# Performance work log

Hardware: AMD Instinct MI355X
Metric: run time of the kernel (lower is better)

Reference implementation:

```python
import jax, jax.numpy as jnp
import numpy as np

B, N, D = 512, 131072, 256
N_BAGS, GRID = 64, 96
DIS_THRESHOLD = 2.0
TEMP = 0.2


def setup_inputs() -> dict:
    key = jax.random.key(0)
    k = jax.random.split(key, 8)
    q = jax.random.normal(k[0], (B, D), dtype=jnp.float32)
    memory = jax.random.normal(k[1], (N, D), dtype=jnp.float32)
    # memory bank holds L2-normalized features (MoCo-style)
    memory = memory / jnp.linalg.norm(memory, axis=1, keepdims=True)
    bag_idx = jax.random.randint(k[2], (B,), 0, N_BAGS, dtype=jnp.int32)
    x_coord = jax.random.randint(k[3], (B,), 0, GRID, dtype=jnp.int32)
    y_coord = jax.random.randint(k[4], (B,), 0, GRID, dtype=jnp.int32)
    bag_idxs = jax.random.randint(k[5], (N,), 0, N_BAGS, dtype=jnp.int32)
    x_coords = jax.random.randint(k[6], (N,), 0, GRID, dtype=jnp.int32)
    y_coords = jax.random.randint(k[7], (N,), 0, GRID, dtype=jnp.int32)
    return {"q": q, "memory": memory, "bag_idx": bag_idx,
            "x_coord": x_coord, "y_coord": y_coord,
            "bag_idxs": bag_idxs, "x_coords": x_coords, "y_coords": y_coords}


def _spatial_pos(q, memory, bag_idx, x_coord, y_coord, bag_idxs, x_coords, y_coords):
    # q = F.normalize(neck(backbone(img))[0])
    qn = q / jnp.linalg.norm(q, axis=1, keepdims=True)
    # l_all = einsum('bc,cn', q, memory.T); s_all = exp(l_all / 0.2)
    l_all = jnp.einsum("bc,nc->bn", qn, memory)  # [B, N]
    s_all = jnp.exp(l_all / TEMP)
    # chosen_patch_idx: same bag as query
    chosen = bag_idx[:, None] == bag_idxs[None, :]  # [B, N] bool
    # cdist(coords, coords_bank, p=2) via squared-distance expansion
    # (coords are small integers -> exact in fp32; compare d^2 against thr^2 / 0)
    cq = jnp.stack((x_coord, y_coord), axis=1).astype(jnp.float32)   # [B, 2]
    cb = jnp.stack((x_coords, y_coords), axis=1).astype(jnp.float32)  # [N, 2]
    d2 = (jnp.sum(cq * cq, axis=1)[:, None]
          + jnp.sum(cb * cb, axis=1)[None, :]
          - 2.0 * cq @ cb.T)  # [B, N]
    near = (d2 < DIS_THRESHOLD * DIS_THRESHOLD) & (d2 > 0.0)
    pos_idx = chosen & near
    # s_pos_spatial = sum(where(pos_idx, s_all, 0), dim=1)
    s_pos_spatial = jnp.sum(jnp.where(pos_idx, s_all, 0.0), axis=1)  # [B]
    return s_pos_spatial, pos_idx


def reference(q, memory, bag_idx, x_coord, y_coord, bag_idxs, x_coords, y_coords):
    s_pos_spatial, _ = _spatial_pos(q, memory, bag_idx, x_coord, y_coord,
                                    bag_idxs, x_coords, y_coords)
    return s_pos_spatial
```

## Files before the change

kernel.cpp:

```cpp
#include <hip/hip_runtime.h>
#include <math.h>

#define NBAGS  64
#define BAGCAP 40
#define TBL    (BAGCAP * NBAGS)
#define D4     64

__global__ void __launch_bounds__(256)
k_fused(const float* __restrict__ q,
        const float* __restrict__ memory,
        const int* __restrict__ bag_idx,
        const int* __restrict__ x_coord,
        const int* __restrict__ y_coord,
        const int* __restrict__ bag_idxs,
        const int* __restrict__ x_coords,
        const int* __restrict__ y_coords,
        float* __restrict__ out,
        int B, int N)
{
    __shared__ int s_cnt[NBAGS];
    __shared__ int s_tbl[TBL];
    int tid = threadIdx.x;
    if (tid < NBAGS) s_cnt[tid] = 0;
    __syncthreads();

    for (int i = tid; i < B; i += 256) {
        int bag  = bag_idx[i];
        int slot = atomicAdd(&s_cnt[bag], 1);
        if (slot < BAGCAP)
            s_tbl[slot * NBAGS + bag] = (i << 14) | (x_coord[i] << 7) | y_coord[i];
    }
    __syncthreads();

    int j = blockIdx.x * 256 + tid;
    if (j >= N) return;

    int jb = bag_idxs[j];
    int jx = x_coords[j];
    int jy = y_coords[j];
    int n  = min(s_cnt[jb], BAGCAP);

    const float4* q4 = (const float4*)q;
    const float4* m4 = (const float4*)memory;

    for (int i = 0; i < n; ++i) {
        int e  = s_tbl[i * NBAGS + jb];
        int dx = ((e >> 7) & 127) - jx;
        int dy = (e & 127) - jy;
        int d2 = dx * dx + dy * dy;
        if (d2 > 0 && d2 < 4) {
            int b = e >> 14;
            const float4* qr = q4 + b * D4;
            const float4* mr = m4 + (long)j * D4;
            float qq = 0.0f, qm = 0.0f;
            #pragma unroll 8
            for (int k = 0; k < D4; ++k) {
                float4 a = qr[k];
                float4 m = mr[k];
                qq += a.x * a.x + a.y * a.y + a.z * a.z + a.w * a.w;
                qm += a.x * m.x + a.y * m.y + a.z * m.z + a.w * m.w;
            }
            float l = qm / sqrtf(qq);
            atomicAdd(&out[b], expf(l * 5.0f));
        }
    }
}

extern "C" void kernel_launch(void* const* d_in, const int* in_sizes, int n_in,
                              void* d_out, int out_size, void* d_ws, size_t ws_size,
                              hipStream_t stream)
{
    const float* q        = (const float*)d_in[0];
    const float* memory   = (const float*)d_in[1];
    const int*   bag_idx  = (const int*)d_in[2];
    const int*   x_coord  = (const int*)d_in[3];
    const int*   y_coord  = (const int*)d_in[4];
    const int*   bag_idxs = (const int*)d_in[5];
    const int*   x_coords = (const int*)d_in[6];
    const int*   y_coords = (const int*)d_in[7];
    float*       out      = (float*)d_out;

    int B = in_sizes[2];
    int N = in_sizes[5];

    hipMemsetAsync(out, 0, (size_t)out_size * sizeof(float), stream);

    int threads = 256;
    int blocks  = (N + threads - 1) / threads;
    k_fused<<<blocks, threads, 0, stream>>>(q, memory, bag_idx, x_coord, y_coord,
                                            bag_idxs, x_coords, y_coords,
                                            out, B, N);
}
```

Before: 202.7 us.

## Compact spatial hits into shared list and compute dot products wave-cooperatively

Matches found by each thread are pushed into a shared-memory hit list (up to 64 per block). After a barrier, each wavefront takes one hit and computes the 256-wide dot product with coalesced float4 loads across its 64 lanes, then reduces with shuffles. This replaces the old scheme in which one thread serially read 256 floats with uncoalesced strided accesses while the rest of its wave sat idle. Hits beyond the list capacity fall back to the old per-thread path. The cost is an extra block-wide barrier and a shared atomic per hit.

```diff
diff --git a/kernel.cpp b/kernel.cpp
--- a/kernel.cpp
+++ b/kernel.cpp
@@ -5,6 +5,7 @@
 #define BAGCAP 40
 #define TBL    (BAGCAP * NBAGS)
 #define D4     64
+#define HITCAP 64
 
 __global__ void __launch_bounds__(256)
 k_fused(const float* __restrict__ q,
@@ -20,8 +21,12 @@
 {
     __shared__ int s_cnt[NBAGS];
     __shared__ int s_tbl[TBL];
+    __shared__ int s_nhit;
+    __shared__ int s_hit[HITCAP];
+
     int tid = threadIdx.x;
     if (tid < NBAGS) s_cnt[tid] = 0;
+    if (tid == NBAGS) s_nhit = 0;
     __syncthreads();
 
     for (int i = tid; i < B; i += 256) {
@@ -32,37 +37,62 @@
     }
     __syncthreads();
 
-    int j = blockIdx.x * 256 + tid;
-    if (j >= N) return;
-
-    int jb = bag_idxs[j];
-    int jx = x_coords[j];
-    int jy = y_coords[j];
-    int n  = min(s_cnt[jb], BAGCAP);
-
     const float4* q4 = (const float4*)q;
     const float4* m4 = (const float4*)memory;
 
-    for (int i = 0; i < n; ++i) {
-        int e  = s_tbl[i * NBAGS + jb];
-        int dx = ((e >> 7) & 127) - jx;
-        int dy = (e & 127) - jy;
-        int d2 = dx * dx + dy * dy;
-        if (d2 > 0 && d2 < 4) {
-            int b = e >> 14;
-            const float4* qr = q4 + b * D4;
-            const float4* mr = m4 + (long)j * D4;
-            float qq = 0.0f, qm = 0.0f;
-            #pragma unroll 8
-            for (int k = 0; k < D4; ++k) {
-                float4 a = qr[k];
-                float4 m = mr[k];
-                qq += a.x * a.x + a.y * a.y + a.z * a.z + a.w * a.w;
-                qm += a.x * m.x + a.y * m.y + a.z * m.z + a.w * m.w;
+    int j = blockIdx.x * 256 + tid;
+    if (j < N) {
+        int jb = bag_idxs[j];
+        int jx = x_coords[j];
+        int jy = y_coords[j];
+        int n  = min(s_cnt[jb], BAGCAP);
+
+        for (int i = 0; i < n; ++i) {
+            int e  = s_tbl[i * NBAGS + jb];
+            int dx = ((e >> 7) & 127) - jx;
+            int dy = (e & 127) - jy;
+            int d2 = dx * dx + dy * dy;
+            if (d2 > 0 && d2 < 4) {
+                int b    = e >> 14;
+                int slot = atomicAdd(&s_nhit, 1);
+                if (slot < HITCAP) {
+                    s_hit[slot] = (j << 9) | b;
+                } else {
+                    const float4* qr = q4 + b * D4;
+                    const float4* mr = m4 + (long)j * D4;
+                    float qq = 0.0f, qm = 0.0f;
+                    #pragma unroll 8
+                    for (int k = 0; k < D4; ++k) {
+                        float4 a = qr[k];
+                        float4 m = mr[k];
+                        qq += a.x * a.x + a.y * a.y + a.z * a.z + a.w * a.w;
+                        qm += a.x * m.x + a.y * m.y + a.z * m.z + a.w * m.w;
+                    }
+                    atomicAdd(&out[b], expf(qm / sqrtf(qq) * 5.0f));
+                }
             }
-            float l = qm / sqrtf(qq);
-            atomicAdd(&out[b], expf(l * 5.0f));
         }
+    }
+    __syncthreads();
+
+    int nh   = min(s_nhit, HITCAP);
+    int wave = tid >> 6;
+    int lane = tid & 63;
+    for (int h = wave; h < nh; h += 4) {
+        int e  = s_hit[h];
+        int b  = e & 511;
+        int jj = e >> 9;
+        float4 a = q4[b * D4 + lane];
+        float4 m = m4[(long)jj * D4 + lane];
+        float qq = a.x * a.x + a.y * a.y + a.z * a.z + a.w * a.w;
+        float qm = a.x * m.x + a.y * m.y + a.z * m.z + a.w * m.w;
+        #pragma unroll
+        for (int mask = 32; mask >= 1; mask >>= 1) {
+            qq += __shfl_xor(qq, mask, 64);
+            qm += __shfl_xor(qm, mask, 64);
+        }
+        if (lane == 0)
+            atomicAdd(&out[b], expf(qm / sqrtf(qq) * 5.0f));
     }
 }
 
```

New measurement: 180.1 us. -11.1%, faster.
